# Optimization experiments

Hardware: AMD Instinct MI355X
Metric: run time of the kernel (lower is better)

The kernel has to match this reference:

```python
import jax, jax.numpy as jnp
import numpy as np

SR = 48000.0
STAB_EPS = 1e-3
BS = 32
N_FRAMES = 128
N_SAMPLES = 65536


def setup_inputs() -> dict:
    key = jax.random.key(0)
    ks = jax.random.split(key, 8)
    f0_hz = jax.random.uniform(ks[0], (BS,), minval=50.0, maxval=500.0)
    note_on_duration = jax.random.uniform(ks[1], (BS,), minval=0.3, maxval=1.0)
    phase = jax.random.uniform(ks[2], (BS,), minval=-np.pi, maxval=np.pi)
    logits = jax.random.normal(ks[3], (BS, N_FRAMES, 5))
    osc_shape = jax.random.uniform(ks[4], (BS,))
    osc_gain = jax.random.uniform(ks[5], (BS,), minval=0.5, maxval=1.0)
    dist_gain = jax.random.uniform(ks[6], (BS,), minval=1.0, maxval=4.0)
    learned_alpha = jax.random.uniform(ks[7], (BS,), minval=0.5, maxval=3.0)
    return dict(f0_hz=f0_hz, note_on_duration=note_on_duration, phase=phase,
                logits=logits, osc_shape=osc_shape, osc_gain=osc_gain,
                dist_gain=dist_gain, learned_alpha=learned_alpha,
                n_samples=N_SAMPLES)


def lin_interp_dim1(x, n_out):
    """Linear interpolation along dim 1 with align_corners=True. x: (bs, n_in, c)."""
    n_in = x.shape[1]
    pos = jnp.linspace(0.0, n_in - 1.0, n_out)
    i0 = jnp.floor(pos).astype(jnp.int32)
    i1 = jnp.minimum(i0 + 1, n_in - 1)
    frac = (pos - i0.astype(x.dtype))[None, :, None]
    return x[:, i0] * (1.0 - frac) + x[:, i1] * frac


def square_saw_vco(f0_hz, osc_shape, n_samples, phase):
    """torchsynth-style square/saw morph oscillator. f0_hz, osc_shape, phase: (bs,)."""
    f0 = f0_hz[:, None]                                   # (bs, 1)
    inc = jnp.broadcast_to(f0 / SR, (f0.shape[0], n_samples))
    arg = 2.0 * jnp.pi * jnp.cumsum(inc, axis=1) + phase[:, None]
    partials = 12000.0 / (f0 * jnp.log10(f0))
    square = jnp.tanh(jnp.pi * partials * jnp.sin(arg) / 2.0)
    s = osc_shape[:, None]
    return (1.0 - s / 2.0) * square * (1.0 + s * jnp.cos(arg / 2.0))


def exp_decay_env(alpha, note_on_duration, n_samples):
    t = jnp.arange(n_samples, dtype=jnp.float32) / SR     # (n,)
    ramp = jnp.clip(1.0 - t[None, :] / note_on_duration[:, None], STAB_EPS, 1.0)
    env = ramp ** alpha[:, None]
    return jnp.where(t[None, :] <= note_on_duration[:, None], env, 0.0)


def logits_to_a_coeff_triangle(a_logits):
    """Map 2 logits to a stable biquad denominator (a1, a2) inside the stability triangle."""
    stab = 1.0 - STAB_EPS
    a1 = 2.0 * jnp.tanh(a_logits[..., 0]) * stab
    a1_abs = jnp.abs(a1)
    a2 = ((2.0 - a1_abs) * jnp.tanh(a_logits[..., 1]) * stab + a1_abs) / 2.0
    return jnp.stack([a1, a2], axis=-1)


def sample_wise_lpc(x, a):
    """Time-varying all-pole order-2: y[t] = x[t] - a1[t]*y[t-1] - a2[t]*y[t-2].
    x: (bs, n), a: (bs, n, 2). Sequential lax.scan over time."""
    def step(carry, inp):
        y1, y2 = carry
        xt, a1, a2 = inp
        y = xt - a1 * y1 - a2 * y2
        return (y, y1), y
    z = jnp.zeros(x.shape[0], dtype=x.dtype)
    xs = (x.T, a[..., 0].T, a[..., 1].T)                  # time-major
    _, ys = jax.lax.scan(step, (z, z), xs)
    return ys.T


def time_varying_fir(x, b):
    """y[t] = b0[t]*x[t] + b1[t]*x[t-1] + b2[t]*x[t-2], zero initial state."""
    x1 = jnp.pad(x, ((0, 0), (1, 0)))[:, :-1]
    x2 = jnp.pad(x, ((0, 0), (2, 0)))[:, :-2]
    return b[..., 0] * x + b[..., 1] * x1 + b[..., 2] * x2


def reference(f0_hz, note_on_duration, phase, logits, osc_shape, osc_gain,
              dist_gain, learned_alpha, n_samples):
    # --- oscillator + envelope ---
    dry = square_saw_vco(f0_hz, osc_shape, n_samples, phase)
    dry = dry * osc_gain[:, None]
    envelope = exp_decay_env(learned_alpha, note_on_duration, n_samples)
    dry = dry * envelope
    # --- coefficients (interp_logits=False: map to coeffs at frame rate, then upsample) ---
    a_coeff = logits_to_a_coeff_triangle(logits[..., :2])   # (bs, n_frames, 2)
    b_coeff = logits[..., 2:]                                # (bs, n_frames, 3)
    a_coeff = lin_interp_dim1(a_coeff, n_samples)            # (bs, n, 2)
    b_coeff = lin_interp_dim1(b_coeff, n_samples)            # (bs, n, 3)
    # --- time-varying biquad: all-pole recursion then FIR ---
    y_a = sample_wise_lpc(dry, a_coeff)
    y_ab = time_varying_fir(y_a, b_coeff)
    # --- distortion ---
    wet = jnp.tanh(y_ab * dist_gain[:, None])
    a0 = jnp.ones_like(a_coeff[:, :, 0])
    a_coeff3 = jnp.stack([a0, a_coeff[:, :, 0], a_coeff[:, :, 1]], axis=2)
    return (dry, wet, envelope, y_ab, a_coeff3, b_coeff, y_a)
```

## Files before the change

### kernel.cpp

```cpp
#include <hip/hip_runtime.h>
#include <cmath>

#define DI __device__ __forceinline__

constexpr int BS = 32;
constexpr int NS = 65536;
constexpr int NF = 128;
constexpr int S  = 4;
constexpr int TB = 256;
constexpr int SAMP = TB * S;
constexpr int NC = NS / SAMP;
constexpr size_t U = (size_t)BS * NS;
constexpr double PI_D = 3.14159265358979323846;
constexpr float STAB = 0.999f;

struct M6 { float a, b, c, d, u, v; };

DI M6 comp(const M6& R, const M6& L) {
    M6 o;
    o.a = fmaf(R.a, L.a, R.b * L.c);
    o.b = fmaf(R.a, L.b, R.b * L.d);
    o.c = fmaf(R.c, L.a, R.d * L.c);
    o.d = fmaf(R.c, L.b, R.d * L.d);
    o.u = fmaf(R.a, L.u, fmaf(R.b, L.v, R.u));
    o.v = fmaf(R.c, L.u, fmaf(R.d, L.v, R.v));
    return o;
}

DI void stepL(M6& A, float a1, float a2, float x) {
    float na = fmaf(-a1, A.a, -a2 * A.c);
    float nb = fmaf(-a1, A.b, -a2 * A.d);
    float nu = fmaf(-a1, A.u, fmaf(-a2, A.v, x));
    A.c = A.a; A.d = A.b; A.v = A.u;
    A.a = na;  A.b = nb;  A.u = nu;
}

DI void wave_scan6(M6& s, int lane) {
    #pragma unroll
    for (int d = 1; d < 64; d <<= 1) {
        M6 o;
        o.a = __shfl_up(s.a, d, 64); o.b = __shfl_up(s.b, d, 64);
        o.c = __shfl_up(s.c, d, 64); o.d = __shfl_up(s.d, d, 64);
        o.u = __shfl_up(s.u, d, 64); o.v = __shfl_up(s.v, d, 64);
        M6 t = comp(s, o);
        bool p = lane >= d;
        s.a = p ? t.a : s.a; s.b = p ? t.b : s.b; s.c = p ? t.c : s.c;
        s.d = p ? t.d : s.d; s.u = p ? t.u : s.u; s.v = p ? t.v : s.v;
    }
}

DI M6 ld6(const float* p) { M6 m; m.a=p[0]; m.b=p[1]; m.c=p[2]; m.d=p[3]; m.u=p[4]; m.v=p[5]; return m; }
DI void st6(float* p, const M6& m) { p[0]=m.a; p[1]=m.b; p[2]=m.c; p[3]=m.d; p[4]=m.u; p[5]=m.v; }

DI void ipos(int t, int& i0, int& i1, float& fr) {
    int pn = t * 127;
    int p0 = pn / 65535;
    i0 = p0;
    i1 = (p0 + 1 > 127) ? 127 : p0 + 1;
    fr = (float)(pn - p0 * 65535) * (1.0f / 65535.0f);
}

DI float fast_tanh(float x) {
    float e = __expf(2.0f * x);
    return 1.0f - 2.0f / (e + 1.0f);
}

DI void stage_frames(const float* __restrict__ logits, int b, int F, int tid,
                     float (*sfa)[2], float (*sfb)[3]) {
    if (tid < 4) {
        int fidx = F + tid; if (fidx > 127) fidx = 127;
        const float* L = logits + (size_t)(b * NF + fidx) * 5;
        float a1 = 2.0f * tanhf(L[0]) * STAB;
        float aa = fabsf(a1);
        float a2 = ((2.0f - aa) * tanhf(L[1]) * STAB + aa) * 0.5f;
        sfa[tid][0] = a1; sfa[tid][1] = a2;
        sfb[tid][0] = L[2]; sfb[tid][1] = L[3]; sfb[tid][2] = L[4];
    }
}

DI void interp4(int t0, int F, const float (*sfa)[2], const float (*sfb)[3],
                float* a1v, float* a2v, float* b0v, float* b1v, float* b2v) {
    #pragma unroll
    for (int k = 0; k < S; k++) {
        int i0, i1; float fr;
        ipos(t0 + k, i0, i1, fr);
        float w0 = 1.0f - fr;
        int l0 = i0 - F, l1 = i1 - F;
        a1v[k] = sfa[l0][0] * w0 + sfa[l1][0] * fr;
        a2v[k] = sfa[l0][1] * w0 + sfa[l1][1] * fr;
        b0v[k] = sfb[l0][0] * w0 + sfb[l1][0] * fr;
        b1v[k] = sfb[l0][1] * w0 + sfb[l1][1] * fr;
        b2v[k] = sfb[l0][2] * w0 + sfb[l1][2] * fr;
    }
}

__global__ __launch_bounds__(TB) void k_osc(
    const float* __restrict__ f0_hz, const float* __restrict__ note_dur,
    const float* __restrict__ phase, const float* __restrict__ logits,
    const float* __restrict__ osc_shape, const float* __restrict__ osc_gain,
    const float* __restrict__ alpha,
    float* __restrict__ ws_chunk, float* __restrict__ out) {
    __shared__ float sfa[4][2], sfb[4][3], wt[4][6];
    __shared__ float sstage[SAMP * 3];
    const int bid = blockIdx.x;
    const int b = bid / NC, c = bid % NC;
    const int tid = threadIdx.x;
    const int t0 = c * SAMP + tid * S;
    const size_t g0 = (size_t)b * NS + t0;
    const int F = (c * SAMP * 127) / 65535;

    stage_frames(logits, b, F, tid, sfa, sfb);

    const float f0 = f0_hz[b];
    const float ph = phase[b];
    const float sh = osc_shape[b];
    const float gn = osc_gain[b];
    const float dur = note_dur[b];
    const float al = alpha[b];
    const double inc = (double)f0 / 48000.0;
    const float partials = 12000.0f / (f0 * __log10f(f0));

    const double cum0 = (double)(t0 + 1) * inc;
    const double uu0 = cum0 - 2.0 * floor(cum0 * 0.5);
    const float theta0 = (float)(PI_D * uu0 + 0.5 * (double)ph);
    const float dth = (float)(PI_D * inc);

    float x[S], env4[S];
    #pragma unroll
    for (int k = 0; k < S; k++) {
        int t = t0 + k;
        float theta = theta0 + (float)k * dth;
        float sn, cs;
        __sincosf(theta, &sn, &cs);
        float sq = fast_tanh(1.57079632679f * partials * (2.0f * sn * cs));
        float dry0 = (1.0f - 0.5f * sh) * sq * (1.0f + sh * cs);
        float tsec = (float)t * (1.0f / 48000.0f);
        float env = 0.0f;
        if (tsec <= dur) {
            float ramp = 1.0f - tsec / dur;
            ramp = ramp < 0.001f ? 0.001f : (ramp > 1.0f ? 1.0f : ramp);
            env = __expf(al * __logf(ramp));
        }
        env4[k] = env;
        x[k] = dry0 * gn * env;
    }
    __syncthreads();

    float a1v[S], a2v[S], b0v[S], b1v[S], b2v[S];
    interp4(t0, F, sfa, sfb, a1v, a2v, b0v, b1v, b2v);

    *(float4*)&out[g0]         = make_float4(x[0], x[1], x[2], x[3]);
    *(float4*)&out[2 * U + g0] = make_float4(env4[0], env4[1], env4[2], env4[3]);

    const int tw = tid * 12;
    const size_t blk0 = ((size_t)b * NS + (size_t)c * SAMP) * 3;
    *(float4*)&sstage[tw + 0] = make_float4(1.0f, a1v[0], a2v[0], 1.0f);
    *(float4*)&sstage[tw + 4] = make_float4(a1v[1], a2v[1], 1.0f, a1v[2]);
    *(float4*)&sstage[tw + 8] = make_float4(a2v[2], 1.0f, a1v[3], a2v[3]);
    __syncthreads();
    {
        float* dst = out + 4 * U + blk0;
        #pragma unroll
        for (int r = 0; r < 3; r++) {
            int wi = r * (TB * 4) + tid * 4;
            *(float4*)&dst[wi] = *(const float4*)&sstage[wi];
        }
    }
    __syncthreads();
    *(float4*)&sstage[tw + 0] = make_float4(b0v[0], b1v[0], b2v[0], b0v[1]);
    *(float4*)&sstage[tw + 4] = make_float4(b1v[1], b2v[1], b0v[2], b1v[2]);
    *(float4*)&sstage[tw + 8] = make_float4(b2v[2], b0v[3], b1v[3], b2v[3]);
    __syncthreads();
    {
        float* dst = out + 7 * U + blk0;
        #pragma unroll
        for (int r = 0; r < 3; r++) {
            int wi = r * (TB * 4) + tid * 4;
            *(float4*)&dst[wi] = *(const float4*)&sstage[wi];
        }
    }

    M6 A; A.a = -a1v[0]; A.b = -a2v[0]; A.c = 1.0f; A.d = 0.0f; A.u = x[0]; A.v = 0.0f;
    #pragma unroll
    for (int k = 1; k < S; k++) stepL(A, a1v[k], a2v[k], x[k]);

    const int lane = tid & 63, w = tid >> 6;
    wave_scan6(A, lane);
    if (lane == 63) st6(wt[w], A);
    __syncthreads();
    if (tid == TB - 1) {
        M6 p = ld6(wt[0]);
        p = comp(ld6(wt[1]), p);
        p = comp(ld6(wt[2]), p);
        M6 tot = comp(A, p);
        st6(ws_chunk + ((size_t)b * NC + c) * 6, tot);
    }
}

__global__ __launch_bounds__(TB) void k_iir(
    const float* __restrict__ logits, const float* __restrict__ dist_gain,
    const float* __restrict__ ws_chunk, float* __restrict__ out) {
    __shared__ float sfa[4][2], sfb[4][3], wt[4][6], sv[NC][2];
    const int bid = blockIdx.x;
    const int b = bid / NC, c = bid % NC;
    const int tid = threadIdx.x;
    const int t0 = c * SAMP + tid * S;
    const size_t g0 = (size_t)b * NS + t0;
    const int F = (c * SAMP * 127) / 65535;

    stage_frames(logits, b, F, tid, sfa, sfb);

    if (tid < NC) {
        M6 cs = ld6(ws_chunk + ((size_t)b * NC + tid) * 6);
        wave_scan6(cs, tid);
        sv[tid][0] = cs.u; sv[tid][1] = cs.v;
    }

    float4 xv = *(const float4*)&out[g0];
    float x[S] = {xv.x, xv.y, xv.z, xv.w};

    __syncthreads();
    const float s0 = c ? sv[c - 1][0] : 0.0f;
    const float s1 = c ? sv[c - 1][1] : 0.0f;

    float a1v[S], a2v[S], b0v[S], b1v[S], b2v[S];
    interp4(t0, F, sfa, sfb, a1v, a2v, b0v, b1v, b2v);

    M6 A; A.a = -a1v[0]; A.b = -a2v[0]; A.c = 1.0f; A.d = 0.0f; A.u = x[0]; A.v = 0.0f;
    #pragma unroll
    for (int k = 1; k < S; k++) stepL(A, a1v[k], a2v[k], x[k]);

    const int lane = tid & 63, w = tid >> 6;
    wave_scan6(A, lane);
    if (lane == 63) st6(wt[w], A);
    __syncthreads();

    M6 P; P.a = 1.f; P.b = 0.f; P.c = 0.f; P.d = 1.f; P.u = 0.f; P.v = 0.f;
    for (int i = 0; i < w; i++) P = comp(ld6(wt[i]), P);
    M6 prev;
    prev.a = __shfl_up(A.a, 1, 64); prev.b = __shfl_up(A.b, 1, 64);
    prev.c = __shfl_up(A.c, 1, 64); prev.d = __shfl_up(A.d, 1, 64);
    prev.u = __shfl_up(A.u, 1, 64); prev.v = __shfl_up(A.v, 1, 64);
    M6 E = (lane == 0) ? P : comp(prev, P);

    float y1 = fmaf(E.a, s0, fmaf(E.b, s1, E.u));
    float y2 = fmaf(E.c, s0, fmaf(E.d, s1, E.v));
    const float ys0 = y1, ys1 = y2;

    float y[S];
    #pragma unroll
    for (int k = 0; k < S; k++) {
        y[k] = fmaf(-a1v[k], y1, fmaf(-a2v[k], y2, x[k]));
        y2 = y1; y1 = y[k];
    }

    const float dg = dist_gain[b];
    float yab[S], wet[S];
    #pragma unroll
    for (int k = 0; k < S; k++) {
        float ym1 = (k >= 1) ? y[k - 1] : ys0;
        float ym2 = (k >= 2) ? y[k - 2] : ((k == 1) ? ys0 : ys1);
        yab[k] = b0v[k] * y[k] + b1v[k] * ym1 + b2v[k] * ym2;
        wet[k] = fast_tanh(yab[k] * dg);
    }

    *(float4*)&out[U + g0]      = make_float4(wet[0], wet[1], wet[2], wet[3]);
    *(float4*)&out[3 * U + g0]  = make_float4(yab[0], yab[1], yab[2], yab[3]);
    *(float4*)&out[10 * U + g0] = make_float4(y[0], y[1], y[2], y[3]);
}

extern "C" void kernel_launch(void* const* d_in, const int* in_sizes, int n_in,
                              void* d_out, int out_size, void* d_ws, size_t ws_size,
                              hipStream_t stream) {
    const float* f0   = (const float*)d_in[0];
    const float* dur  = (const float*)d_in[1];
    const float* ph   = (const float*)d_in[2];
    const float* lg   = (const float*)d_in[3];
    const float* shp  = (const float*)d_in[4];
    const float* gn   = (const float*)d_in[5];
    const float* dist = (const float*)d_in[6];
    const float* alp  = (const float*)d_in[7];
    float* out = (float*)d_out;
    float* ws_chunk = (float*)d_ws;

    k_osc<<<BS * NC, TB, 0, stream>>>(f0, dur, ph, lg, shp, gn, alp, ws_chunk, out);
    k_iir<<<BS * NC, TB, 0, stream>>>(lg, dist, ws_chunk, out);
}
```

Baseline: 125.0 us.

## Recompute oscillator in IIR pass, use DPP wave scan and nontemporal stores

The IIR kernel now recomputes the dry oscillator and envelope samples instead of re-reading the dry output written by the first kernel, which removes one full-size global read. The 64-lane scan replaces __shfl_up with DPP row shifts and row broadcasts to cut the cost of cross-lane data movement. All large output writes become nontemporal stores so they do not pollute the cache. In exchange the transcendental oscillator math runs twice, and the recomputed values must match the stored dry output bit for bit.

```diff
diff --git a/kernel.cpp b/kernel.cpp
--- a/kernel.cpp
+++ b/kernel.cpp
@@ -14,6 +14,10 @@
 constexpr double PI_D = 3.14159265358979323846;
 constexpr float STAB = 0.999f;
 
+typedef float f4 __attribute__((ext_vector_type(4)));
+DI f4 mkf4(float a, float b, float c, float d) { f4 r; r.x=a; r.y=b; r.z=c; r.w=d; return r; }
+DI void ntst4(const f4 v, float* p) { __builtin_nontemporal_store(v, (f4*)p); }
+
 struct M6 { float a, b, c, d, u, v; };
 
 DI M6 comp(const M6& R, const M6& L) {
@@ -35,18 +39,29 @@
     A.a = na;  A.b = nb;  A.u = nu;
 }
 
+template<int CTRL> DI float dppf(float x) {
+    return __int_as_float(__builtin_amdgcn_update_dpp(
+        __float_as_int(x), __float_as_int(x), CTRL, 0xF, 0xF, false));
+}
+template<int CTRL> DI M6 dpp6(const M6& s) {
+    M6 o;
+    o.a = dppf<CTRL>(s.a); o.b = dppf<CTRL>(s.b);
+    o.c = dppf<CTRL>(s.c); o.d = dppf<CTRL>(s.d);
+    o.u = dppf<CTRL>(s.u); o.v = dppf<CTRL>(s.v);
+    return o;
+}
+DI void sel6(M6& s, const M6& t, bool p) {
+    s.a = p ? t.a : s.a; s.b = p ? t.b : s.b; s.c = p ? t.c : s.c;
+    s.d = p ? t.d : s.d; s.u = p ? t.u : s.u; s.v = p ? t.v : s.v;
+}
 DI void wave_scan6(M6& s, int lane) {
-    #pragma unroll
-    for (int d = 1; d < 64; d <<= 1) {
-        M6 o;
-        o.a = __shfl_up(s.a, d, 64); o.b = __shfl_up(s.b, d, 64);
-        o.c = __shfl_up(s.c, d, 64); o.d = __shfl_up(s.d, d, 64);
-        o.u = __shfl_up(s.u, d, 64); o.v = __shfl_up(s.v, d, 64);
-        M6 t = comp(s, o);
-        bool p = lane >= d;
-        s.a = p ? t.a : s.a; s.b = p ? t.b : s.b; s.c = p ? t.c : s.c;
-        s.d = p ? t.d : s.d; s.u = p ? t.u : s.u; s.v = p ? t.v : s.v;
-    }
+    const int sub = lane & 15;
+    { M6 o = dpp6<0x111>(s); M6 t = comp(s, o); sel6(s, t, sub >= 1); }
+    { M6 o = dpp6<0x112>(s); M6 t = comp(s, o); sel6(s, t, sub >= 2); }
+    { M6 o = dpp6<0x114>(s); M6 t = comp(s, o); sel6(s, t, sub >= 4); }
+    { M6 o = dpp6<0x118>(s); M6 t = comp(s, o); sel6(s, t, sub >= 8); }
+    { M6 o = dpp6<0x142>(s); M6 t = comp(s, o); sel6(s, t, (lane & 16) != 0); }
+    { M6 o = dpp6<0x143>(s); M6 t = comp(s, o); sel6(s, t, lane >= 32); }
 }
 
 DI M6 ld6(const float* p) { M6 m; m.a=p[0]; m.b=p[1]; m.c=p[2]; m.d=p[3]; m.u=p[4]; m.v=p[5]; return m; }
@@ -94,38 +109,14 @@
     }
 }
 
-__global__ __launch_bounds__(TB) void k_osc(
-    const float* __restrict__ f0_hz, const float* __restrict__ note_dur,
-    const float* __restrict__ phase, const float* __restrict__ logits,
-    const float* __restrict__ osc_shape, const float* __restrict__ osc_gain,
-    const float* __restrict__ alpha,
-    float* __restrict__ ws_chunk, float* __restrict__ out) {
-    __shared__ float sfa[4][2], sfb[4][3], wt[4][6];
-    __shared__ float sstage[SAMP * 3];
-    const int bid = blockIdx.x;
-    const int b = bid / NC, c = bid % NC;
-    const int tid = threadIdx.x;
-    const int t0 = c * SAMP + tid * S;
-    const size_t g0 = (size_t)b * NS + t0;
-    const int F = (c * SAMP * 127) / 65535;
-
-    stage_frames(logits, b, F, tid, sfa, sfb);
-
-    const float f0 = f0_hz[b];
-    const float ph = phase[b];
-    const float sh = osc_shape[b];
-    const float gn = osc_gain[b];
-    const float dur = note_dur[b];
-    const float al = alpha[b];
+DI void osc4(int t0, float f0, float ph, float sh, float gn, float dur, float al,
+             float* x, float* env4) {
     const double inc = (double)f0 / 48000.0;
     const float partials = 12000.0f / (f0 * __log10f(f0));
-
     const double cum0 = (double)(t0 + 1) * inc;
     const double uu0 = cum0 - 2.0 * floor(cum0 * 0.5);
     const float theta0 = (float)(PI_D * uu0 + 0.5 * (double)ph);
     const float dth = (float)(PI_D * inc);
-
-    float x[S], env4[S];
     #pragma unroll
     for (int k = 0; k < S; k++) {
         int t = t0 + k;
@@ -144,39 +135,61 @@
         env4[k] = env;
         x[k] = dry0 * gn * env;
     }
+}
+
+__global__ __launch_bounds__(TB) void k_osc(
+    const float* __restrict__ f0_hz, const float* __restrict__ note_dur,
+    const float* __restrict__ phase, const float* __restrict__ logits,
+    const float* __restrict__ osc_shape, const float* __restrict__ osc_gain,
+    const float* __restrict__ alpha,
+    float* __restrict__ ws_chunk, float* __restrict__ out) {
+    __shared__ float sfa[4][2], sfb[4][3], wt[4][6];
+    __shared__ float sstage[SAMP * 3];
+    const int bid = blockIdx.x;
+    const int b = bid / NC, c = bid % NC;
+    const int tid = threadIdx.x;
+    const int t0 = c * SAMP + tid * S;
+    const size_t g0 = (size_t)b * NS + t0;
+    const int F = (c * SAMP * 127) / 65535;
+
+    stage_frames(logits, b, F, tid, sfa, sfb);
+
+    float x[S], env4[S];
+    osc4(t0, f0_hz[b], phase[b], osc_shape[b], osc_gain[b], note_dur[b], alpha[b],
+         x, env4);
     __syncthreads();
 
     float a1v[S], a2v[S], b0v[S], b1v[S], b2v[S];
     interp4(t0, F, sfa, sfb, a1v, a2v, b0v, b1v, b2v);
 
-    *(float4*)&out[g0]         = make_float4(x[0], x[1], x[2], x[3]);
-    *(float4*)&out[2 * U + g0] = make_float4(env4[0], env4[1], env4[2], env4[3]);
+    ntst4(mkf4(x[0], x[1], x[2], x[3]), &out[g0]);
+    ntst4(mkf4(env4[0], env4[1], env4[2], env4[3]), &out[2 * U + g0]);
 
     const int tw = tid * 12;
     const size_t blk0 = ((size_t)b * NS + (size_t)c * SAMP) * 3;
-    *(float4*)&sstage[tw + 0] = make_float4(1.0f, a1v[0], a2v[0], 1.0f);
-    *(float4*)&sstage[tw + 4] = make_float4(a1v[1], a2v[1], 1.0f, a1v[2]);
-    *(float4*)&sstage[tw + 8] = make_float4(a2v[2], 1.0f, a1v[3], a2v[3]);
+    *(f4*)&sstage[tw + 0] = mkf4(1.0f, a1v[0], a2v[0], 1.0f);
+    *(f4*)&sstage[tw + 4] = mkf4(a1v[1], a2v[1], 1.0f, a1v[2]);
+    *(f4*)&sstage[tw + 8] = mkf4(a2v[2], 1.0f, a1v[3], a2v[3]);
     __syncthreads();
     {
         float* dst = out + 4 * U + blk0;
         #pragma unroll
         for (int r = 0; r < 3; r++) {
             int wi = r * (TB * 4) + tid * 4;
-            *(float4*)&dst[wi] = *(const float4*)&sstage[wi];
+            ntst4(*(const f4*)&sstage[wi], &dst[wi]);
         }
     }
     __syncthreads();
-    *(float4*)&sstage[tw + 0] = make_float4(b0v[0], b1v[0], b2v[0], b0v[1]);
-    *(float4*)&sstage[tw + 4] = make_float4(b1v[1], b2v[1], b0v[2], b1v[2]);
-    *(float4*)&sstage[tw + 8] = make_float4(b2v[2], b0v[3], b1v[3], b2v[3]);
+    *(f4*)&sstage[tw + 0] = mkf4(b0v[0], b1v[0], b2v[0], b0v[1]);
+    *(f4*)&sstage[tw + 4] = mkf4(b1v[1], b2v[1], b0v[2], b1v[2]);
+    *(f4*)&sstage[tw + 8] = mkf4(b2v[2], b0v[3], b1v[3], b2v[3]);
     __syncthreads();
     {
         float* dst = out + 7 * U + blk0;
         #pragma unroll
         for (int r = 0; r < 3; r++) {
             int wi = r * (TB * 4) + tid * 4;
-            *(float4*)&dst[wi] = *(const float4*)&sstage[wi];
+            ntst4(*(const f4*)&sstage[wi], &dst[wi]);
         }
     }
 
@@ -198,7 +211,10 @@
 }
 
 __global__ __launch_bounds__(TB) void k_iir(
-    const float* __restrict__ logits, const float* __restrict__ dist_gain,
+    const float* __restrict__ f0_hz, const float* __restrict__ note_dur,
+    const float* __restrict__ phase, const float* __restrict__ logits,
+    const float* __restrict__ osc_shape, const float* __restrict__ osc_gain,
+    const float* __restrict__ dist_gain, const float* __restrict__ alpha,
     const float* __restrict__ ws_chunk, float* __restrict__ out) {
     __shared__ float sfa[4][2], sfb[4][3], wt[4][6], sv[NC][2];
     const int bid = blockIdx.x;
@@ -216,8 +232,9 @@
         sv[tid][0] = cs.u; sv[tid][1] = cs.v;
     }
 
-    float4 xv = *(const float4*)&out[g0];
-    float x[S] = {xv.x, xv.y, xv.z, xv.w};
+    float x[S], env4[S];
+    osc4(t0, f0_hz[b], phase[b], osc_shape[b], osc_gain[b], note_dur[b], alpha[b],
+         x, env4);
 
     __syncthreads();
     const float s0 = c ? sv[c - 1][0] : 0.0f;
@@ -264,9 +281,9 @@
         wet[k] = fast_tanh(yab[k] * dg);
     }
 
-    *(float4*)&out[U + g0]      = make_float4(wet[0], wet[1], wet[2], wet[3]);
-    *(float4*)&out[3 * U + g0]  = make_float4(yab[0], yab[1], yab[2], yab[3]);
-    *(float4*)&out[10 * U + g0] = make_float4(y[0], y[1], y[2], y[3]);
+    ntst4(mkf4(wet[0], wet[1], wet[2], wet[3]), &out[U + g0]);
+    ntst4(mkf4(yab[0], yab[1], yab[2], yab[3]), &out[3 * U + g0]);
+    ntst4(mkf4(y[0], y[1], y[2], y[3]), &out[10 * U + g0]);
 }
 
 extern "C" void kernel_launch(void* const* d_in, const int* in_sizes, int n_in,
@@ -284,5 +301,5 @@
     float* ws_chunk = (float*)d_ws;
 
     k_osc<<<BS * NC, TB, 0, stream>>>(f0, dur, ph, lg, shp, gn, alp, ws_chunk, out);
-    k_iir<<<BS * NC, TB, 0, stream>>>(lg, dist, ws_chunk, out);
-}
+    k_iir<<<BS * NC, TB, 0, stream>>>(f0, dur, ph, lg, shp, gn, dist, alp, ws_chunk, out);
+}
```

After: 129.5 us. 3.6% more time.
